# Performance work log

Hardware: AMD Instinct MI355X
Metric: run time of the kernel (lower is better)

## Reference

```python
import jax, jax.numpy as jnp
import numpy as np

B, T, N, H, O = 32, 512, 512, 1024, 512
K = H  # default CirculantHH: kernel_size = hidden_dim
PAD_LEFT = K // 2  # F.pad circular left amount used in CirculantHH.forward


def setup_inputs() -> dict:
    key = jax.random.key(0)
    ks = jax.random.split(key, 7)
    x = jax.random.normal(ks[0], (B, T, N), dtype=jnp.float32)
    h0 = jax.random.normal(ks[1], (1, B, H), dtype=jnp.float32)
    # input_linear params (nn.Linear default-ish scale)
    Wi = jax.random.normal(ks[2], (H, N), dtype=jnp.float32) / np.sqrt(N)
    bi = jax.random.normal(ks[3], (H,), dtype=jnp.float32) * 0.01
    # output_linear params
    Wo = jax.random.normal(ks[4], (O, H), dtype=jnp.float32) / np.sqrt(H)
    bo = jax.random.normal(ks[5], (O,), dtype=jnp.float32) * 0.01
    # circulant kernel (first "correlation" taps, length K=H), small scale like
    # a Fro-projected circulant (target ||w||_2 = target_fro/sqrt(H) = 1/sqrt(3H))
    w = jax.random.normal(ks[6], (K,), dtype=jnp.float32)
    w = w / jnp.linalg.norm(w) * (1.0 / np.sqrt(3.0 * H))
    return {"x": x, "h0": h0, "Wi": Wi, "bi": bi, "Wo": Wo, "bo": bo, "w": w}


def _circulant_matrix(w):
    # y[i] = sum_k w[k] * h[(i - PAD_LEFT + k) mod H]  (Conv1d correlation after
    # circular pad). Equivalent matrix C with y = h @ C.T:
    i = jnp.arange(H)[:, None]
    j = jnp.arange(H)[None, :]
    idx = (j - i + PAD_LEFT) % H  # k index such that column j contributes w[k]
    return w[idx]  # (H, H)


def reference(x, h0, Wi, bi, Wo, bo, w):
    C = _circulant_matrix(w)  # (H, H)
    h_init = h0[0]  # (B, H)
    x_proj = jnp.einsum('btn,hn->bth', x, Wi) + bi  # precompute input projection

    def step(h, xp_t):
        pre = xp_t + h @ C.T  # (B, H)
        h_new = jnp.tanh(pre)
        return h_new, h_new

    _, z_seq = jax.lax.scan(step, h_init, jnp.swapaxes(x_proj, 0, 1))  # (T, B, H)
    z_seq = jnp.swapaxes(z_seq, 0, 1)  # (B, T, H)
    logits = jnp.einsum('bth,oh->bto', z_seq, Wo) + bo
    out = jax.nn.softmax(logits, axis=2)
    return out, z_seq
```

## Files before the change

kernel.cpp:

```cpp
#include <hip/hip_runtime.h>

#define B_ 32
#define T_ 512
#define N_ 512
#define H_ 1024
#define O_ 512

typedef _Float16 h4 __attribute__((ext_vector_type(4)));
typedef _Float16 h8 __attribute__((ext_vector_type(8)));
typedef float f4 __attribute__((ext_vector_type(4)));

__device__ __forceinline__ float tanh_fast(float x) {
  return 1.f - 2.f / (__expf(2.f * x) + 1.f);
}

__device__ __forceinline__ f4 mfma32(h8 a, h8 b, f4 c) {
#if defined(__has_builtin) && __has_builtin(__builtin_amdgcn_mfma_f32_16x16x32_f16)
  return __builtin_amdgcn_mfma_f32_16x16x32_f16(a, b, c, 0, 0, 0);
#else
  asm volatile("v_mfma_f32_16x16x32_f16 %0, %1, %2, %0"
               : "+v"(c) : "v"(a), "v"(b));
  return c;
#endif
}

template <typename OutT>
__global__ __launch_bounds__(256, 2)
void gemm_bt_k32(const float* __restrict__ A, const float* __restrict__ Bt,
                 const float* __restrict__ bias, OutT* __restrict__ C,
                 int M, int N, int K) {
  __shared__ __align__(16) _Float16 As[128 * 40];
  __shared__ __align__(16) _Float16 Bs[128 * 40];
  const int tid = threadIdx.x;
  const int m0 = blockIdx.x * 128;
  const int n0 = blockIdx.y * 128;
  const int lane = tid & 63;
  const int wv = tid >> 6;
  const int ln15 = lane & 15;
  const int lq = lane >> 4;
  const int mw = (wv >> 1) * 64;
  const int nw = (wv & 1) * 64;

  f4 acc[4][4];
#pragma unroll
  for (int mi = 0; mi < 4; ++mi)
#pragma unroll
    for (int ni = 0; ni < 4; ++ni) acc[mi][ni] = (f4){0.f, 0.f, 0.f, 0.f};

  for (int k0 = 0; k0 < K; k0 += 32) {
#pragma unroll
    for (int r = 0; r < 4; ++r) {
      const int q = tid + r * 256;
      const int row = q >> 3;
      const int cq = q & 7;
      const int p = 8 * (cq & 3) + 4 * (cq >> 2);
      const float4 av =
          *reinterpret_cast<const float4*>(&A[(size_t)(m0 + row) * K + k0 + cq * 4]);
      h4 af;
      af.x = (_Float16)av.x; af.y = (_Float16)av.y;
      af.z = (_Float16)av.z; af.w = (_Float16)av.w;
      *reinterpret_cast<h4*>(&As[row * 40 + p]) = af;
      const float4 bv =
          *reinterpret_cast<const float4*>(&Bt[(size_t)(n0 + row) * K + k0 + cq * 4]);
      h4 bf;
      bf.x = (_Float16)bv.x; bf.y = (_Float16)bv.y;
      bf.z = (_Float16)bv.z; bf.w = (_Float16)bv.w;
      *reinterpret_cast<h4*>(&Bs[row * 40 + p]) = bf;
    }
    __syncthreads();

    h8 af[4], bf[4];
#pragma unroll
    for (int mi = 0; mi < 4; ++mi)
      af[mi] = *reinterpret_cast<const h8*>(&As[(mw + mi * 16 + ln15) * 40 + 8 * lq]);
#pragma unroll
    for (int ni = 0; ni < 4; ++ni)
      bf[ni] = *reinterpret_cast<const h8*>(&Bs[(nw + ni * 16 + ln15) * 40 + 8 * lq]);
#pragma unroll
    for (int mi = 0; mi < 4; ++mi)
#pragma unroll
      for (int ni = 0; ni < 4; ++ni)
        acc[mi][ni] = mfma32(af[mi], bf[ni], acc[mi][ni]);
    __syncthreads();
  }

#pragma unroll
  for (int ni = 0; ni < 4; ++ni) {
    const int n = n0 + nw + ni * 16 + ln15;
    const float bv = bias[n];
#pragma unroll
    for (int mi = 0; mi < 4; ++mi) {
      const int mbase = m0 + mw + mi * 16 + 4 * lq;
#pragma unroll
      for (int r = 0; r < 4; ++r)
        C[(size_t)(mbase + r) * N + n] = (OutT)(acc[mi][ni][r] + bv);
    }
  }
}

#define HS 1040

template <int XPF16>
__global__ __launch_bounds__(512, 2)
void elman_mfma(const void* __restrict__ xp_, float* __restrict__ z,
                const float* __restrict__ h0, const float* __restrict__ w,
                int L, int W) {
  __shared__ __align__(16) _Float16 wB[64 * 64 * 8];
  __shared__ __align__(16) _Float16 hbuf[2][16 * HS];

  const int blk = blockIdx.x;
  const int bg = blk & 1;
  const int c = blk >> 1;
  const int t0 = c * L;
  const int tstart = (c == 0) ? 0 : max(0, t0 - W);
  const int tend = t0 + L;

  const int tid = threadIdx.x;
  const int lane = tid & 63;
  const int ln15 = lane & 15;
  const int lq = lane >> 4;
  const int j0 = 8 * (tid >> 6);

  for (int idx = tid; idx < 4096; idx += 512) {
    const int p = idx >> 6, ln = idx & 63;
    const int base = 16 * p + 4 * (ln >> 4) - (ln & 15) + 512;
    h8 f;
#pragma unroll
    for (int e = 0; e < 8; ++e)
      f[e] = (_Float16)w[(base + 16 * (e >> 2) + (e & 3)) & 1023];
    reinterpret_cast<h8*>(wB)[idx] = f;
  }

  for (int i = tid; i < 16 * 1024; i += 512) {
    const int row = i >> 10, col = i & 1023;
    const int ph =
        32 * (col >> 5) + 8 * ((col >> 2) & 3) + 4 * ((col >> 4) & 1) + (col & 3);
    hbuf[0][row * HS + ph] =
        (c == 0) ? (_Float16)h0[(bg * 16 + row) * H_ + col] : (_Float16)0.f;
  }
  __syncthreads();

  const h8* tab = reinterpret_cast<const h8*>(wB);

  int pp = 0;
  for (int t = tstart; t < tend; ++t) {
    float xv[8][4];
#pragma unroll
    for (int jj = 0; jj < 8; ++jj) {
      const int j = 16 * (j0 + jj) + ln15;
#pragma unroll
      for (int r = 0; r < 4; ++r) {
        const int brow = 4 * lq + r;
        const size_t gi = ((size_t)(bg * 16 + brow) * T_ + t) * H_ + j;
        if constexpr (XPF16)
          xv[jj][r] = (float)((const _Float16*)xp_)[gi];
        else
          xv[jj][r] = ((const float*)xp_)[gi];
      }
    }
    __builtin_amdgcn_sched_barrier(0);

    const _Float16* hr = &hbuf[pp][0];
    const int abase = ln15 * HS + 8 * lq;

    f4 acc[8];
#pragma unroll
    for (int jj = 0; jj < 8; ++jj) acc[jj] = (f4){0.f, 0.f, 0.f, 0.f};

    h8 Bw[10];
#pragma unroll
    for (int k = 0; k < 8; ++k) {
      const int u = 57 + k;
      Bw[u % 10] = tab[((u - j0) & 63) * 64 + lane];
    }
    h8 Acur = *reinterpret_cast<const h8*>(hr + abase);

#pragma unroll
    for (int b = 0; b < 32; ++b) {
      if (b < 31) {
        const int u1 = 2 * b + 65, u2 = 2 * b + 66;
        Bw[u1 % 10] = tab[((u1 - j0) & 63) * 64 + lane];
        Bw[u2 % 10] = tab[((u2 - j0) & 63) * 64 + lane];
      }
      h8 Anext = Acur;
      if (b < 31)
        Anext = *reinterpret_cast<const h8*>(hr + abase + 32 * (b + 1));
#pragma unroll
      for (int jj = 0; jj < 8; ++jj) {
        const int u = 2 * b - jj + 64;
        acc[jj] = mfma32(Acur, Bw[u % 10], acc[jj]);
      }
      Acur = Anext;
    }

    _Float16* hw = &hbuf[pp ^ 1][0];
#pragma unroll
    for (int jj = 0; jj < 8; ++jj) {
      const int J = j0 + jj;
      const int j = 16 * J + ln15;
      const int ph = 32 * (J >> 1) + 8 * (ln15 >> 2) + 4 * (J & 1) + (ln15 & 3);
#pragma unroll
      for (int r = 0; r < 4; ++r) {
        const int brow = 4 * lq + r;
        const float hn = tanh_fast(xv[jj][r] + acc[jj][r]);
        if (t >= t0)
          z[((size_t)(bg * 16 + brow) * T_ + t) * H_ + j] = hn;
        hw[brow * HS + ph] = (_Float16)hn;
      }
    }
    pp ^= 1;
    __syncthreads();
  }
}

__global__ __launch_bounds__(256)
void softmax_rows(float* __restrict__ out, int rows) {
  const int row = blockIdx.x * 4 + (threadIdx.x >> 6);
  if (row >= rows) return;
  const int lane = threadIdx.x & 63;
  float* p = out + (size_t)row * O_;

  float4 v0 = *(float4*)&p[lane * 4];
  float4 v1 = *(float4*)&p[256 + lane * 4];

  float m = fmaxf(fmaxf(fmaxf(v0.x, v0.y), fmaxf(v0.z, v0.w)),
                  fmaxf(fmaxf(v1.x, v1.y), fmaxf(v1.z, v1.w)));
#pragma unroll
  for (int off = 32; off > 0; off >>= 1) m = fmaxf(m, __shfl_xor(m, off));

  v0.x = __expf(v0.x - m);
  v0.y = __expf(v0.y - m);
  v0.z = __expf(v0.z - m);
  v0.w = __expf(v0.w - m);
  v1.x = __expf(v1.x - m);
  v1.y = __expf(v1.y - m);
  v1.z = __expf(v1.z - m);
  v1.w = __expf(v1.w - m);

  float s = ((v0.x + v0.y) + (v0.z + v0.w)) + ((v1.x + v1.y) + (v1.z + v1.w));
#pragma unroll
  for (int off = 32; off > 0; off >>= 1) s += __shfl_xor(s, off);

  const float inv = 1.f / s;
  v0.x *= inv; v0.y *= inv; v0.z *= inv; v0.w *= inv;
  v1.x *= inv; v1.y *= inv; v1.z *= inv; v1.w *= inv;
  *(float4*)&p[lane * 4] = v0;
  *(float4*)&p[256 + lane * 4] = v1;
}

extern "C" void kernel_launch(void* const* d_in, const int* in_sizes, int n_in,
                              void* d_out, int out_size, void* d_ws, size_t ws_size,
                              hipStream_t stream) {
  const float* x  = (const float*)d_in[0];
  const float* h0 = (const float*)d_in[1];
  const float* Wi = (const float*)d_in[2];
  const float* bi = (const float*)d_in[3];
  const float* Wo = (const float*)d_in[4];
  const float* bo = (const float*)d_in[5];
  const float* w  = (const float*)d_in[6];

  float* out = (float*)d_out;
  float* z   = out + (size_t)B_ * T_ * O_;

  const size_t xp_bytes = (size_t)B_ * T_ * H_ * sizeof(_Float16);
  const bool chunked = (ws_size >= xp_bytes);

  if (chunked) {
    _Float16* xp = (_Float16*)d_ws;
    gemm_bt_k32<_Float16><<<dim3((B_ * T_) / 128, H_ / 128), 256, 0, stream>>>(
        x, Wi, bi, xp, B_ * T_, H_, N_);
    const int L = 4, W = 3;
    elman_mfma<1><<<2 * (T_ / L), 512, 0, stream>>>(xp, z, h0, w, L, W);
  } else {
    gemm_bt_k32<float><<<dim3((B_ * T_) / 128, H_ / 128), 256, 0, stream>>>(
        x, Wi, bi, z, B_ * T_, H_, N_);
    elman_mfma<0><<<2, 512, 0, stream>>>(z, z, h0, w, T_, 0);
  }

  gemm_bt_k32<float><<<dim3((B_ * T_) / 128, O_ / 128), 256, 0, stream>>>(
      z, Wo, bo, out, B_ * T_, O_, H_);

  softmax_rows<<<(B_ * T_) / 4, 256, 0, stream>>>(out, B_ * T_);
}
```

Baseline: 165.0 us.

## Double-buffer shared tiles with register prefetch in projection GEMM

Converts the GEMM main loop to a two-stage pipeline. Shared-memory tiles are double-buffered, and the next K-tile's global loads are issued into registers while the current tile's MFMAs run. This hides global-load latency and allows one barrier per iteration instead of two. The cost is double the LDS footprint and extra registers, which may reduce occupancy under the launch bounds.

```diff
diff --git a/kernel.cpp b/kernel.cpp
--- a/kernel.cpp
+++ b/kernel.cpp
@@ -29,8 +29,8 @@
 void gemm_bt_k32(const float* __restrict__ A, const float* __restrict__ Bt,
                  const float* __restrict__ bias, OutT* __restrict__ C,
                  int M, int N, int K) {
-  __shared__ __align__(16) _Float16 As[128 * 40];
-  __shared__ __align__(16) _Float16 Bs[128 * 40];
+  __shared__ __align__(16) _Float16 As[2][128 * 40];
+  __shared__ __align__(16) _Float16 Bs[2][128 * 40];
   const int tid = threadIdx.x;
   const int m0 = blockIdx.x * 128;
   const int n0 = blockIdx.y * 128;
@@ -41,41 +41,79 @@
   const int mw = (wv >> 1) * 64;
   const int nw = (wv & 1) * 64;
 
+  int srow[4], scol[4], sp[4];
+#pragma unroll
+  for (int r = 0; r < 4; ++r) {
+    const int q = tid + r * 256;
+    srow[r] = q >> 3;
+    const int cq = q & 7;
+    scol[r] = cq * 4;
+    sp[r] = 8 * (cq & 3) + 4 * (cq >> 2);
+  }
+
   f4 acc[4][4];
 #pragma unroll
   for (int mi = 0; mi < 4; ++mi)
 #pragma unroll
     for (int ni = 0; ni < 4; ++ni) acc[mi][ni] = (f4){0.f, 0.f, 0.f, 0.f};
 
-  for (int k0 = 0; k0 < K; k0 += 32) {
+  float4 rA[4], rB[4];
+#pragma unroll
+  for (int r = 0; r < 4; ++r) {
+    rA[r] = *reinterpret_cast<const float4*>(&A[(size_t)(m0 + srow[r]) * K + scol[r]]);
+    rB[r] = *reinterpret_cast<const float4*>(&Bt[(size_t)(n0 + srow[r]) * K + scol[r]]);
+  }
+#pragma unroll
+  for (int r = 0; r < 4; ++r) {
+    h4 af, bf;
+    af.x = (_Float16)rA[r].x; af.y = (_Float16)rA[r].y;
+    af.z = (_Float16)rA[r].z; af.w = (_Float16)rA[r].w;
+    *reinterpret_cast<h4*>(&As[0][srow[r] * 40 + sp[r]]) = af;
+    bf.x = (_Float16)rB[r].x; bf.y = (_Float16)rB[r].y;
+    bf.z = (_Float16)rB[r].z; bf.w = (_Float16)rB[r].w;
+    *reinterpret_cast<h4*>(&Bs[0][srow[r] * 40 + sp[r]]) = bf;
+  }
+  const int NT = K >> 5;
+  if (NT > 1) {
 #pragma unroll
     for (int r = 0; r < 4; ++r) {
-      const int q = tid + r * 256;
-      const int row = q >> 3;
-      const int cq = q & 7;
-      const int p = 8 * (cq & 3) + 4 * (cq >> 2);
-      const float4 av =
-          *reinterpret_cast<const float4*>(&A[(size_t)(m0 + row) * K + k0 + cq * 4]);
-      h4 af;
-      af.x = (_Float16)av.x; af.y = (_Float16)av.y;
-      af.z = (_Float16)av.z; af.w = (_Float16)av.w;
-      *reinterpret_cast<h4*>(&As[row * 40 + p]) = af;
-      const float4 bv =
-          *reinterpret_cast<const float4*>(&Bt[(size_t)(n0 + row) * K + k0 + cq * 4]);
-      h4 bf;
-      bf.x = (_Float16)bv.x; bf.y = (_Float16)bv.y;
-      bf.z = (_Float16)bv.z; bf.w = (_Float16)bv.w;
-      *reinterpret_cast<h4*>(&Bs[row * 40 + p]) = bf;
-    }
-    __syncthreads();
-
+      rA[r] = *reinterpret_cast<const float4*>(&A[(size_t)(m0 + srow[r]) * K + 32 + scol[r]]);
+      rB[r] = *reinterpret_cast<const float4*>(&Bt[(size_t)(n0 + srow[r]) * K + 32 + scol[r]]);
+    }
+  }
+  __syncthreads();
+
+  for (int t = 0; t < NT; ++t) {
+    const int cur = t & 1;
     h8 af[4], bf[4];
 #pragma unroll
     for (int mi = 0; mi < 4; ++mi)
-      af[mi] = *reinterpret_cast<const h8*>(&As[(mw + mi * 16 + ln15) * 40 + 8 * lq]);
+      af[mi] = *reinterpret_cast<const h8*>(&As[cur][(mw + mi * 16 + ln15) * 40 + 8 * lq]);
 #pragma unroll
     for (int ni = 0; ni < 4; ++ni)
-      bf[ni] = *reinterpret_cast<const h8*>(&Bs[(nw + ni * 16 + ln15) * 40 + 8 * lq]);
+      bf[ni] = *reinterpret_cast<const h8*>(&Bs[cur][(nw + ni * 16 + ln15) * 40 + 8 * lq]);
+
+    if (t + 1 < NT) {
+#pragma unroll
+      for (int r = 0; r < 4; ++r) {
+        h4 afh, bfh;
+        afh.x = (_Float16)rA[r].x; afh.y = (_Float16)rA[r].y;
+        afh.z = (_Float16)rA[r].z; afh.w = (_Float16)rA[r].w;
+        *reinterpret_cast<h4*>(&As[cur ^ 1][srow[r] * 40 + sp[r]]) = afh;
+        bfh.x = (_Float16)rB[r].x; bfh.y = (_Float16)rB[r].y;
+        bfh.z = (_Float16)rB[r].z; bfh.w = (_Float16)rB[r].w;
+        *reinterpret_cast<h4*>(&Bs[cur ^ 1][srow[r] * 40 + sp[r]]) = bfh;
+      }
+      if (t + 2 < NT) {
+        const int k0 = (t + 2) * 32;
+#pragma unroll
+        for (int r = 0; r < 4; ++r) {
+          rA[r] = *reinterpret_cast<const float4*>(&A[(size_t)(m0 + srow[r]) * K + k0 + scol[r]]);
+          rB[r] = *reinterpret_cast<const float4*>(&Bt[(size_t)(n0 + srow[r]) * K + k0 + scol[r]]);
+        }
+      }
+    }
+
 #pragma unroll
     for (int mi = 0; mi < 4; ++mi)
 #pragma unroll
```

Measured after the change: 152.1 us. 7.8% less time.
